# Performance work log

Hardware: AMD Instinct MI355X
Metric: run time of the kernel (lower is better)

The kernel has to match this reference:

```python
import jax, jax.numpy as jnp
import numpy as np

B, C, H, S, E, NH, DD, DS = 16, 256, 1024, 1024, 512, 8, 512, 64
HD = E // NH               # head dim = 64
REL_MAX = 2048             # seq_len + prediction_length
S1 = S + 1                 # dyn tokens + 1 static token
NEG = jnp.float32(-1e9)


def setup_inputs() -> dict:
    key = jax.random.key(0)
    ks = jax.random.split(key, 24)
    rn = lambda k, shp, s=0.02: (jax.random.normal(k, shp, jnp.float32) * s)
    return {
        # forward tensor args
        "x":      jax.random.normal(ks[0], (B, C, H), jnp.float32),
        "dyn":    jax.random.normal(ks[1], (B, S, DD), jnp.float32),
        "static": jax.random.normal(ks[2], (B, DS), jnp.float32),
        # dynamic/static encoders (nn.Linear: y = x @ W.T + b)
        "dyn_W":  rn(ks[3], (E, DD)),  "dyn_b":  jnp.zeros((E,), jnp.float32),
        "stat_W": rn(ks[4], (E, DS)),  "stat_b": jnp.zeros((E,), jnp.float32),
        # static FiLM MLP: Linear(E,E) -> LeakyReLU(0.1) -> Linear(E,C) -> Tanh
        "film_W1": rn(ks[5], (E, E)), "film_b1": jnp.zeros((E,), jnp.float32),
        "film_W2": rn(ks[6], (C, E)), "film_b2": jnp.zeros((C,), jnp.float32),
        # query_proj: Conv1d(C->E, k=1)  (weight stored as [E, C])
        "q_W": rn(ks[7], (E, C)), "q_b": jnp.zeros((E,), jnp.float32),
        # MultiheadAttention packed in-proj [3E, E] and out-proj [E, E]
        "in_proj_W": rn(ks[8], (3 * E, E)), "in_proj_b": jnp.zeros((3 * E,), jnp.float32),
        "out_W": rn(ks[9], (E, E)), "out_b": jnp.zeros((E,), jnp.float32),
        # context_proj: Conv1d(E->C, k=1) (weight stored as [C, E])
        "ctx_W": rn(ks[10], (C, E)), "ctx_b": jnp.zeros((C,), jnp.float32),
        # learned relative-position bias table, size 2*REL_MAX-1
        "bias_table": rn(ks[11], (2 * REL_MAX - 1,)),
    }


def _leaky(v):
    return jnp.where(v >= 0, v, 0.1 * v)


def _attn_mask(bias_table):
    """Fused relative-position bias + causal mask, shape [H, S1]."""
    q_ids = jnp.arange(H)[:, None]           # [H,1]
    k_ids = jnp.arange(S1)[None, :]          # [1,S1]
    rel = jnp.clip(q_ids - k_ids, -REL_MAX + 1, REL_MAX - 1)
    bias = bias_table[rel + REL_MAX - 1]     # [H,S1]
    # dynamic tokens: query q may attend dyn token j only if j <= min(q, S-1);
    # last (static) token always visible
    allowed = jnp.minimum(q_ids, S - 1)
    blocked = (k_ids < S) & (k_ids > allowed)
    return bias + jnp.where(blocked, NEG, 0.0)


def reference(x, dyn, static, dyn_W, dyn_b, stat_W, stat_b,
              film_W1, film_b1, film_W2, film_b2, q_W, q_b,
              in_proj_W, in_proj_b, out_W, out_b, ctx_W, ctx_b, bias_table):
    # encoders
    dyn_tokens = dyn @ dyn_W.T + dyn_b                      # [B,S,E]
    static_token = static @ stat_W.T + stat_b               # [B,E]
    film = jnp.tanh(_leaky(static_token @ film_W1.T + film_b1) @ film_W2.T + film_b2)  # [B,C]
    cond_tokens = jnp.concatenate([dyn_tokens, static_token[:, None, :]], axis=1)      # [B,S1,E]

    # query_proj (1x1 conv) : [B,C,H] -> [B,H,E]
    query = jnp.einsum('bch,ec->bhe', x, q_W) + q_b

    # multi-head cross-attention with additive mask
    Wq, Wk, Wv = in_proj_W[:E], in_proj_W[E:2 * E], in_proj_W[2 * E:]
    bq, bk, bv = in_proj_b[:E], in_proj_b[E:2 * E], in_proj_b[2 * E:]
    q = (query @ Wq.T + bq).reshape(B, H, NH, HD).transpose(0, 2, 1, 3)        # [B,NH,H,HD]
    k = (cond_tokens @ Wk.T + bk).reshape(B, S1, NH, HD).transpose(0, 2, 1, 3)  # [B,NH,S1,HD]
    v = (cond_tokens @ Wv.T + bv).reshape(B, S1, NH, HD).transpose(0, 2, 1, 3)

    mask = _attn_mask(bias_table)                                               # [H,S1]
    scores = jnp.einsum('bnqd,bnkd->bnqk', q, k) / jnp.sqrt(jnp.float32(HD)) + mask
    attn = jax.nn.softmax(scores, axis=-1)
    ctx = jnp.einsum('bnqk,bnkd->bnqd', attn, v)                                # [B,NH,H,HD]
    ctx = ctx.transpose(0, 2, 1, 3).reshape(B, H, E) @ out_W.T + out_b          # [B,H,E]

    cond_context = jnp.swapaxes(ctx, 1, 2)                                      # [B,E,H]
    cond_residual = jnp.einsum('beh,ce->bch', cond_context, ctx_W) + ctx_b[None, :, None]
    scale = (1.0 + film)[:, :, None]                                            # FiLM [B,C,1]
    x_cond = (x + cond_residual) * scale                                        # == x*s + res*s
    return x_cond
```

## Files before the change

kernel.cpp:

```cpp
#include <hip/hip_runtime.h>
#include <cmath>

#define B_  16
#define C_  256
#define H_  1024
#define S_  1024
#define E_  512
#define NH_ 8
#define DD_ 512
#define DS_ 64
#define HD_ 64
#define S1_ 1025
#define RELM 2048
#define SV  1032

typedef __attribute__((ext_vector_type(8))) short bf16x8;
typedef __attribute__((ext_vector_type(4))) float f32x4;

__device__ __forceinline__ unsigned short f2bf(float f) {
    unsigned u = __float_as_uint(f);
    u += 0x7fffu + ((u >> 16) & 1u);
    return (unsigned short)(u >> 16);
}

#if __has_builtin(__builtin_amdgcn_exp2f)
#define EXP2F(x) __builtin_amdgcn_exp2f(x)
#else
#define EXP2F(x) exp2f(x)
#endif

__device__ __forceinline__ void gl2lds16(const unsigned short* g, unsigned short* l) {
#if __has_builtin(__builtin_amdgcn_global_load_lds)
    __builtin_amdgcn_global_load_lds(
        (const __attribute__((address_space(1))) void*)g,
        (__attribute__((address_space(3))) void*)l, 16, 0, 0);
#else
    const int ln = threadIdx.x & 63;
    *(bf16x8*)(l + ln * 8) = *(const bf16x8*)g;
#endif
}

__device__ __forceinline__ void conv8(const float* __restrict__ src,
                                      unsigned short* __restrict__ dst, int i) {
    float4 a = *(const float4*)(src + i);
    float4 b = *(const float4*)(src + i + 4);
    bf16x8 o;
    ((unsigned short*)&o)[0] = f2bf(a.x); ((unsigned short*)&o)[1] = f2bf(a.y);
    ((unsigned short*)&o)[2] = f2bf(a.z); ((unsigned short*)&o)[3] = f2bf(a.w);
    ((unsigned short*)&o)[4] = f2bf(b.x); ((unsigned short*)&o)[5] = f2bf(b.y);
    ((unsigned short*)&o)[6] = f2bf(b.z); ((unsigned short*)&o)[7] = f2bf(b.w);
    *(bf16x8*)(dst + i) = o;
}

__device__ __forceinline__ float wred(float p) {
#pragma unroll
    for (int off = 32; off; off >>= 1) p += __shfl_down(p, off, 64);
    return p;
}

#define U_DYN 1048576
#define U_KV  1114112
#define U_Q   1146880
#define U_TOT 1163264
__global__ __launch_bounds__(512)
void prep_conv(const float* __restrict__ dyn, unsigned short* __restrict__ dyn16,
               const float* __restrict__ ipW, unsigned short* __restrict__ ipWq16,
               unsigned short* __restrict__ ipWkv16,
               const float* __restrict__ ctxW, unsigned short* __restrict__ ctxW16,
               const float* __restrict__ statIn,
               const float* __restrict__ stat_W, const float* __restrict__ stat_b,
               float* __restrict__ st_g, unsigned short* __restrict__ st16,
               const float* __restrict__ x, unsigned short* __restrict__ xT)
{
    __shared__ float tle[64][65];
    const int blk = blockIdx.x;
    const int t = threadIdx.x;
    if (blk < 512) {
        const float* ipWkv = ipW + (size_t)E_ * E_;
        const int stride = 512 * 512;
        for (int u = blk * 512 + t; u < U_TOT; u += stride) {
            if (u < U_DYN)      conv8(dyn,   dyn16,   u * 8);
            else if (u < U_KV)  conv8(ipWkv, ipWkv16, (u - U_DYN) * 8);
            else if (u < U_Q)   conv8(ipW,   ipWq16,  (u - U_KV) * 8);
            else                conv8(ctxW,  ctxW16,  (u - U_Q) * 8);
        }
    } else if (blk < 576) {
        const int sub = blk - 512;
        const int b = sub >> 2;
        const int q = sub & 3;
        const int wv = t >> 6;
        const int ln = t & 63;
        const float sv = statIn[b * DS_ + ln];
#pragma unroll 4
        for (int i = 0; i < 16; i++) {
            const int r = q * 128 + wv * 16 + i;
            const float p = wred(stat_W[(size_t)r * DS_ + ln] * sv);
            if (ln == 0) {
                const float v = p + stat_b[r];
                st_g[(size_t)b * E_ + r] = v;
                st16[(size_t)b * E_ + r] = f2bf(v);
            }
        }
    } else {
        const int sub = blk - 576;
        const int b  = sub >> 6;
        const int c0 = ((sub >> 4) & 3) * 64;
        const int h0 = (sub & 15) * 64;
        const int tx = t & 15, ty = t >> 4;
#pragma unroll
        for (int i = 0; i < 2; i++) {
            const float4 v = *(const float4*)&x[((size_t)(b * C_ + c0 + ty + i * 32)) * H_ + h0 + tx * 4];
            tle[ty + i * 32][tx * 4 + 0] = v.x;
            tle[ty + i * 32][tx * 4 + 1] = v.y;
            tle[ty + i * 32][tx * 4 + 2] = v.z;
            tle[ty + i * 32][tx * 4 + 3] = v.w;
        }
        __syncthreads();
#pragma unroll
        for (int i = 0; i < 2; i++) {
            const int hh = ty + i * 32;
            ushort4 o;
            o.x = f2bf(tle[tx * 4 + 0][hh]);
            o.y = f2bf(tle[tx * 4 + 1][hh]);
            o.z = f2bf(tle[tx * 4 + 2][hh]);
            o.w = f2bf(tle[tx * 4 + 3][hh]);
            *(ushort4*)&xT[((size_t)(b * H_ + h0 + hh)) * C_ + c0 + tx * 4] = o;
        }
    }
}

__global__ __launch_bounds__(512)
void prep_misc(const float* __restrict__ ipW, const float* __restrict__ ipb,
               const float* __restrict__ ctxW,
               const float* __restrict__ q_W, unsigned short* __restrict__ qWT16,
               const float* __restrict__ dynW, unsigned short* __restrict__ dynWT16,
               const float* __restrict__ outW, unsigned short* __restrict__ outWT16,
               const float* __restrict__ q_b, float* __restrict__ qb2,
               const float* __restrict__ dyn_b, float* __restrict__ bkv2,
               const float* __restrict__ out_b, const float* __restrict__ ctx_b,
               float* __restrict__ cb2,
               const float* __restrict__ st_g,
               const float* __restrict__ fW1, const float* __restrict__ fb1,
               float* __restrict__ h1_g)
{
    __shared__ float tle[64][65];
    const int blk = blockIdx.x;
    const int t = threadIdx.x;
    const float* ipWkv = ipW + (size_t)E_ * E_;
    const float* ipbkv = ipb + E_;

    if (blk < 128) {
        const int b   = blk >> 3;
        const int oct = blk & 7;
        const int wv  = t >> 6;
        const int ln  = t & 63;
        float str[8];
        *(float4*)&str[0] = *(const float4*)&st_g[(size_t)b * E_ + ln * 8];
        *(float4*)&str[4] = *(const float4*)&st_g[(size_t)b * E_ + ln * 8 + 4];
#pragma unroll 2
        for (int i = 0; i < 8; i++) {
            const int r = oct * 64 + wv * 8 + i;
            const float* wr = fW1 + (size_t)r * E_ + ln * 8;
            const float4 a = *(const float4*)wr;
            const float4 c = *(const float4*)(wr + 4);
            float p = a.x * str[0] + a.y * str[1] + a.z * str[2] + a.w * str[3]
                    + c.x * str[4] + c.y * str[5] + c.z * str[6] + c.w * str[7];
            p = wred(p);
            if (ln == 0) {
                const float v = p + fb1[r];
                h1_g[(size_t)b * E_ + r] = (v >= 0.f) ? v : 0.1f * v;
            }
        }
    } else if (blk < 352) {
        const int row = (blk - 128) * 8 + (t >> 6);
        const int ln  = t & 63;
        const float* src; const float* vec; float bias; float* dst;
        if (row < 512)       { src = ipW + (size_t)row * E_;            vec = q_b;   bias = ipb[row];        dst = qb2 + row; }
        else if (row < 1536) { const int n = row - 512;  src = ipWkv + (size_t)n * E_; vec = dyn_b; bias = ipbkv[n]; dst = bkv2 + n; }
        else                 { const int n = row - 1536; src = ctxW + (size_t)n * E_;  vec = out_b; bias = ctx_b[n]; dst = cb2 + n; }
        const float4 a  = *(const float4*)(src + ln * 8);
        const float4 c  = *(const float4*)(src + ln * 8 + 4);
        const float4 va = *(const float4*)(vec + ln * 8);
        const float4 vc = *(const float4*)(vec + ln * 8 + 4);
        float p = a.x * va.x + a.y * va.y + a.z * va.z + a.w * va.w
                + c.x * vc.x + c.y * vc.y + c.z * vc.z + c.w * vc.w;
        p = wred(p);
        if (ln == 0) *dst = p + bias;
    } else {
        const float* src; unsigned short* dst; int R, Cc, tile;
        const int tt = blk - 352;
        if (tt < 32)      { src = q_W;  dst = qWT16;   R = 512; Cc = 256; tile = tt; }
        else if (tt < 96) { src = dynW; dst = dynWT16; R = 512; Cc = 512; tile = tt - 32; }
        else              { src = outW; dst = outWT16; R = 512; Cc = 512; tile = tt - 96; }
        const int tpr = Cc / 64;
        const int r0 = (tile / tpr) * 64;
        const int c0 = (tile % tpr) * 64;
        const int tx = t & 15, ty = t >> 4;
#pragma unroll
        for (int i = 0; i < 2; i++) {
            const float4 v = *(const float4*)&src[(size_t)(r0 + ty + i * 32) * Cc + c0 + tx * 4];
            tle[ty + i * 32][tx * 4 + 0] = v.x;
            tle[ty + i * 32][tx * 4 + 1] = v.y;
            tle[ty + i * 32][tx * 4 + 2] = v.z;
            tle[ty + i * 32][tx * 4 + 3] = v.w;
        }
        __syncthreads();
#pragma unroll
        for (int i = 0; i < 2; i++) {
            const int cc = ty + i * 32;
            ushort4 o;
            o.x = f2bf(tle[tx * 4 + 0][cc]);
            o.y = f2bf(tle[tx * 4 + 1][cc]);
            o.z = f2bf(tle[tx * 4 + 2][cc]);
            o.w = f2bf(tle[tx * 4 + 3][cc]);
            *(ushort4*)&dst[(size_t)(c0 + cc) * R + r0 + tx * 4] = o;
        }
    }
}

__global__ __launch_bounds__(256)
void gemm_fold3(const unsigned short* __restrict__ ipWq16, const unsigned short* __restrict__ qWT16,
                unsigned short* __restrict__ WqW16,
                const unsigned short* __restrict__ ipWkv16, const unsigned short* __restrict__ dynWT16,
                unsigned short* __restrict__ Wkv216,
                const unsigned short* __restrict__ ctxW16, const unsigned short* __restrict__ outWT16,
                unsigned short* __restrict__ M216,
                const float* __restrict__ h1_g,
                const float* __restrict__ fW2, const float* __restrict__ fb2,
                float* __restrict__ scaleB)
{
    __shared__ unsigned short At[128 * 32];
    __shared__ unsigned short Wt[128 * 32];
    const int bid = blockIdx.x;
    const int tid  = threadIdx.x;
    if (bid >= 48) {
        const int sub = bid - 48;
        const int b = sub >> 2;
        const int q = sub & 3;
        const int wv = tid >> 6;
        const int ln = tid & 63;
        float h1r[8];
        *(float4*)&h1r[0] = *(const float4*)&h1_g[(size_t)b * E_ + ln * 8];
        *(float4*)&h1r[4] = *(const float4*)&h1_g[(size_t)b * E_ + ln * 8 + 4];
#pragma unroll 2
        for (int i = 0; i < 16; i++) {
            const int c = q * 64 + wv * 16 + i;
            const float* wr = fW2 + (size_t)c * E_ + ln * 8;
            const float4 a = *(const float4*)wr;
            const float4 cc = *(const float4*)(wr + 4);
            float p = a.x * h1r[0] + a.y * h1r[1] + a.z * h1r[2] + a.w * h1r[3]
                    + cc.x * h1r[4] + cc.y * h1r[5] + cc.z * h1r[6] + cc.w * h1r[7];
            p = wred(p);
            if (ln == 0) scaleB[b * C_ + c] = 1.f + tanhf(p + fb2[c]);
        }
        return;
    }
    const unsigned short *A, *W; unsigned short* O; int N, mb, nb;
    if (bid < 8)       { A = ipWq16;  W = qWT16;   O = WqW16;  N = 256; mb = bid >> 1;       nb = bid & 1; }
    else if (bid < 40) { A = ipWkv16; W = dynWT16; O = Wkv216; N = 512; mb = (bid - 8) >> 2; nb = (bid - 8) & 3; }
    else               { A = ctxW16;  W = outWT16; O = M216;   N = 512; mb = (bid - 40) >> 2; nb = (bid - 40) & 3; }
    const int m0 = mb * 128, n0 = nb * 128;

    const int wave = tid >> 6;
    const int lane = tid & 63;
    const int quad = lane >> 4;
    const int l15  = lane & 15;
    const int rw = (wave >> 1) * 64;
    const int cw = (wave & 1) * 64;
    const int srow = lane >> 2;
    const int scol = (lane & 3) * 8;

    f32x4 acc[4][4] = {};
    for (int k0 = 0; k0 < 512; k0 += 32) {
        __syncthreads();
#pragma unroll
        for (int c = 0; c < 2; c++) {
            const int chunk = wave + c * 4;
            gl2lds16(A + (size_t)(m0 + chunk * 16 + srow) * 512 + k0 + scol, &At[chunk * 512]);
            gl2lds16(W + (size_t)(n0 + chunk * 16 + srow) * 512 + k0 + scol, &Wt[chunk * 512]);
        }
        __syncthreads();
        bf16x8 af[4], wf[4];
#pragma unroll
        for (int i = 0; i < 4; i++)
            af[i] = *(const bf16x8*)&At[(rw + i * 16 + l15) * 32 + quad * 8];
#pragma unroll
        for (int j = 0; j < 4; j++)
            wf[j] = *(const bf16x8*)&Wt[(cw + j * 16 + l15) * 32 + quad * 8];
#pragma unroll
        for (int i = 0; i < 4; i++)
#pragma unroll
            for (int j = 0; j < 4; j++)
                acc[i][j] = __builtin_amdgcn_mfma_f32_16x16x32_bf16(af[i], wf[j], acc[i][j], 0, 0, 0);
    }
#pragma unroll
    for (int i = 0; i < 4; i++)
#pragma unroll
        for (int r = 0; r < 4; r++) {
            const int mm = m0 + rw + i * 16 + quad * 4 + r;
            unsigned short* cp = O + (size_t)mm * N + n0 + cw + l15;
#pragma unroll
            for (int j = 0; j < 4; j++)
                cp[j * 16] = f2bf(acc[i][j][r]);
        }
}

__global__ __launch_bounds__(256)
void gemm_qkv(const unsigned short* __restrict__ xT16, const unsigned short* __restrict__ WqW16,
              const float* __restrict__ qb2, unsigned short* __restrict__ q16,
              const unsigned short* __restrict__ dynA, const unsigned short* __restrict__ stA,
              const unsigned short* __restrict__ Wdyn, const unsigned short* __restrict__ Wst,
              const float* __restrict__ bdyn, const float* __restrict__ bst,
              unsigned short* __restrict__ k16, unsigned short* __restrict__ vtmp)
{
    __shared__ unsigned short At[2][128 * 32];
    __shared__ unsigned short Wt[2][128 * 32];
    const int bid0 = blockIdx.x;
    const int t = (bid0 & 7) * 193 + (bid0 >> 3);

    const int tid  = threadIdx.x;
    const int wave = tid >> 6;
    const int lane = tid & 63;
    const int quad = lane >> 4;
    const int l15  = lane & 15;
    const int rw = (wave >> 1) * 64;
    const int cw = (wave & 1) * 64;
    const int srow = lane >> 2;
    const int scol = (lane & 3) * 8;

    const unsigned short *A, *W;
    int m0, n0, K;
    bool isQ, stat = false;
    if (t < 1032) {
        const int y = t >> 3;
        stat = (y == 128);
        A = stat ? stA : dynA;
        W = stat ? Wst : Wdyn;
        m0 = stat ? 0 : y * 128;
        n0 = (t & 7) * 128;
        K = 512; isQ = false;
    } else {
        const int u = t - 1032;
        A = xT16; W = WqW16;
        m0 = (u >> 2) * 128;
        n0 = (u & 3) * 128;
        K = 256; isQ = true;
    }

    f32x4 acc[4][4] = {};
#pragma unroll
    for (int c = 0; c < 2; c++) {
        const int chunk = wave + c * 4;
        gl2lds16(A + (size_t)(m0 + chunk * 16 + srow) * K + scol, &At[0][chunk * 512]);
        gl2lds16(W + (size_t)(n0 + chunk * 16 + srow) * K + scol, &Wt[0][chunk * 512]);
    }
    int cur = 0;
    for (int k0 = 0; k0 < K; k0 += 32) {
        __syncthreads();
        if (k0 + 32 < K) {
            const int kn = k0 + 32;
#pragma unroll
            for (int c = 0; c < 2; c++) {
                const int chunk = wave + c * 4;
                gl2lds16(A + (size_t)(m0 + chunk * 16 + srow) * K + kn + scol, &At[cur ^ 1][chunk * 512]);
                gl2lds16(W + (size_t)(n0 + chunk * 16 + srow) * K + kn + scol, &Wt[cur ^ 1][chunk * 512]);
            }
        }
        bf16x8 af[4], wf[4];
#pragma unroll
        for (int i = 0; i < 4; i++)
            af[i] = *(const bf16x8*)&At[cur][(rw + i * 16 + l15) * 32 + quad * 8];
#pragma unroll
        for (int j = 0; j < 4; j++)
            wf[j] = *(const bf16x8*)&Wt[cur][(cw + j * 16 + l15) * 32 + quad * 8];
#pragma unroll
        for (int i = 0; i < 4; i++)
#pragma unroll
            for (int j = 0; j < 4; j++)
                acc[i][j] = __builtin_amdgcn_mfma_f32_16x16x32_bf16(af[i], wf[j], acc[i][j], 0, 0, 0);
        cur ^= 1;
    }

    if (isQ) {
        float bias4[4];
#pragma unroll
        for (int j = 0; j < 4; j++) bias4[j] = qb2[n0 + cw + j * 16 + l15];
#pragma unroll
        for (int i = 0; i < 4; i++) {
#pragma unroll
            for (int r = 0; r < 4; r++) {
                const int mm = m0 + rw + i * 16 + quad * 4 + r;
                unsigned short* cp = q16 + (size_t)mm * 512 + n0 + cw + l15;
#pragma unroll
                for (int j = 0; j < 4; j++)
                    cp[j * 16] = f2bf(acc[i][j][r] + bias4[j]);
            }
        }
    } else {
        const float* bias = stat ? bst : bdyn;
        const bool isV = (n0 >= 512);
        unsigned short* base = isV ? vtmp : k16;
        const int c0 = (isV ? n0 - 512 : n0) + cw + l15;
        float bias4[4];
#pragma unroll
        for (int j = 0; j < 4; j++) bias4[j] = bias[n0 + cw + j * 16 + l15];
#pragma unroll
        for (int i = 0; i < 4; i++) {
#pragma unroll
            for (int r = 0; r < 4; r++) {
                const int am = m0 + rw + i * 16 + quad * 4 + r;
                if (!stat || am < 16) {
                    const int orow = stat ? (am * S1_ + S_) : ((am >> 10) * S1_ + (am & 1023));
                    unsigned short* cp = base + (size_t)orow * 512 + c0;
#pragma unroll
                    for (int j = 0; j < 4; j++)
                        cp[j * 16] = f2bf(acc[i][j][r] + bias4[j]);
                }
            }
        }
    }
}

__global__ __launch_bounds__(256)
void gemm_final(const unsigned short* __restrict__ A, const unsigned short* __restrict__ W,
                const float* __restrict__ bias, float* __restrict__ Cout,
                const float* __restrict__ x, const float* __restrict__ scale)
{
    __shared__ unsigned short At[64 * 32];
    __shared__ unsigned short Wt[128 * 32];
    const int tid  = threadIdx.x;
    const int wave = tid >> 6;
    const int lane = tid & 63;
    const int quad = lane >> 4;
    const int l15  = lane & 15;
    const int m0 = blockIdx.y * 64;
    const int n0 = blockIdx.x * 128;
    const int rw = (wave >> 1) * 32;
    const int cw = (wave & 1) * 64;
    const int zb = blockIdx.z;
    const unsigned short* Wb = W + (size_t)zb * H_ * E_;

    const int srow = lane >> 2;
    const int scol = (lane & 3) * 8;

    f32x4 acc[2][4] = {};

    for (int k0 = 0; k0 < E_; k0 += 32) {
        __syncthreads();
        gl2lds16(A  + (size_t)(m0 + wave * 16 + srow) * E_ + k0 + scol, &At[wave * 512]);
#pragma unroll
        for (int c = 0; c < 2; c++) {
            const int chunk = wave + c * 4;
            gl2lds16(Wb + (size_t)(n0 + chunk * 16 + srow) * E_ + k0 + scol, &Wt[chunk * 512]);
        }
        __syncthreads();
        bf16x8 af[2], wf[4];
#pragma unroll
        for (int i = 0; i < 2; i++)
            af[i] = *(const bf16x8*)&At[(rw + i * 16 + l15) * 32 + quad * 8];
#pragma unroll
        for (int j = 0; j < 4; j++)
            wf[j] = *(const bf16x8*)&Wt[(cw + j * 16 + l15) * 32 + quad * 8];
#pragma unroll
        for (int i = 0; i < 2; i++)
#pragma unroll
            for (int j = 0; j < 4; j++)
                acc[i][j] = __builtin_amdgcn_mfma_f32_16x16x32_bf16(af[i], wf[j], acc[i][j], 0, 0, 0);
    }

#pragma unroll
    for (int i = 0; i < 2; i++) {
#pragma unroll
        for (int r = 0; r < 4; r++) {
            const int mm = m0 + rw + i * 16 + quad * 4 + r;
            const float cb = bias[mm];
            const float sc = scale[zb * C_ + mm];
            const size_t base = ((size_t)(zb * C_ + mm)) * H_ + n0 + cw + l15;
#pragma unroll
            for (int j = 0; j < 4; j++)
                Cout[base + j * 16] = (x[base + j * 16] + acc[i][j][r] + cb) * sc;
        }
    }
}

__global__ __launch_bounds__(256)
void vtrans_kernel(const unsigned short* __restrict__ vtmp, unsigned short* __restrict__ vT)
{
    __shared__ unsigned short tle[64][72];
    const int b = blockIdx.z;
    const int s0 = blockIdx.x * 64;
    const int d0 = blockIdx.y * 64;
    const int tx = threadIdx.x & 15;
    const int ty = threadIdx.x >> 4;
#pragma unroll
    for (int i = 0; i < 4; i++) {
        const int s = s0 + ty + i * 16;
        ushort4 v = {0, 0, 0, 0};
        if (s < S1_)
            v = *(const ushort4*)&vtmp[((size_t)(b * S1_ + s)) * 512 + d0 + tx * 4];
        tle[ty + i * 16][tx * 4 + 0] = v.x;
        tle[ty + i * 16][tx * 4 + 1] = v.y;
        tle[ty + i * 16][tx * 4 + 2] = v.z;
        tle[ty + i * 16][tx * 4 + 3] = v.w;
    }
    __syncthreads();
    if (s0 + tx * 4 < SV) {
#pragma unroll
        for (int i = 0; i < 4; i++) {
            const int dd = ty + i * 16;
            ushort4 o;
            o.x = tle[tx * 4 + 0][dd];
            o.y = tle[tx * 4 + 1][dd];
            o.z = tle[tx * 4 + 2][dd];
            o.w = tle[tx * 4 + 3][dd];
            *(ushort4*)&vT[((size_t)(b * 512 + d0 + dd)) * SV + s0 + tx * 4] = o;
        }
    }
}

#define KS 72
#define VTS 40
#define PS 40

__global__ __launch_bounds__(256)
void attn_mfma_kernel(const unsigned short* __restrict__ q,
                      const unsigned short* __restrict__ k16,
                      const unsigned short* __restrict__ vT,
                      const float* __restrict__ bt,
                      unsigned short* __restrict__ ctx)
{
    const int blk  = blockIdx.x;
    const int qt   = 7 - (blk >> 7);
    const int pair = blk & 127;
    const int nh   = pair & 7;
    const int b    = pair >> 3;
    const int tid  = threadIdx.x;
    const int wave = tid >> 6;
    const int lane = tid & 63;
    const int quad = lane >> 4;
    const int l15  = lane & 15;
    const int q0w  = qt * 128 + wave * 32;

    __shared__ unsigned short Kt[32 * KS];
    __shared__ unsigned short VTl[64 * VTS];
    __shared__ unsigned short Pt[4][16 * PS];
    __shared__ float btl[2048];

    for (int i = tid; i < 2048; i += 256)
        btl[i] = (i < 1024) ? -1.0e9f : bt[1023 + i] * 1.442695041f;

    const float c2 = 0.125f * 1.442695041f;

    bf16x8 qa[2][2];
    const size_t qbase = ((size_t)(b * H_ + q0w)) * E_ + nh * HD_;
#pragma unroll
    for (int qf = 0; qf < 2; qf++)
#pragma unroll
        for (int ch = 0; ch < 2; ch++)
            qa[qf][ch] = *(const bf16x8*)(q + qbase + (size_t)(qf * 16 + l15) * E_ + ch * 32 + quad * 8);

    bf16x8 ones;
#pragma unroll
    for (int j = 0; j < 8; j++) ((short*)&ones)[j] = (short)0x3F80;

    f32x4 o[2][4] = {};
    f32x4 lf[2] = {};
    bf16x8 pa[2];

    const int srow = tid >> 3;
    const int scol = (tid & 7) * 8;
    const int frow = tid >> 2;
    const int fcol = (tid & 3) * 8;
    const unsigned short* kbase = k16 + (size_t)(b * S1_) * 512 + nh * HD_;
    const unsigned short* vrow = vT + ((size_t)(b * 512 + nh * HD_ + frow)) * SV;
    const int ntiles = 4 * qt + 5;
    const int wblk0 = (l15 >> 3);
    const int wsub  = (l15 & 7);
    const int rblk  = (quad ^ ((l15 >> 2) & 3)) << 3;

    bf16x8 kreg = *(const bf16x8*)(kbase + (size_t)srow * 512 + scol);
    bf16x8 vreg = *(const bf16x8*)(vrow + fcol);

    for (int t = 0; t < ntiles; t++) {
        const int k0 = (t == ntiles - 1) ? 1024 : t * 32;
        __syncthreads();
        {
            *(bf16x8*)&Kt[srow * KS + scol] = kreg;
            *(bf16x8*)&VTl[frow * VTS + fcol] = vreg;
        }
        __syncthreads();
        if (t + 1 < ntiles) {
            const int nk0 = (t + 1 == ntiles - 1) ? 1024 : (t + 1) * 32;
            kreg = *(const bf16x8*)(kbase + (size_t)(nk0 + srow) * 512 + scol);
            vreg = *(const bf16x8*)(vrow + nk0 + fcol);
        }

        f32x4 s[2][2] = {};
        __builtin_amdgcn_s_setprio(1);
#pragma unroll
        for (int ch = 0; ch < 2; ch++) {
            const bf16x8 kb0 = *(const bf16x8*)&Kt[l15 * KS + ch * 32 + quad * 8];
            const bf16x8 kb1 = *(const bf16x8*)&Kt[(16 + l15) * KS + ch * 32 + quad * 8];
            s[0][0] = __builtin_amdgcn_mfma_f32_16x16x32_bf16(qa[0][ch], kb0, s[0][0], 0, 0, 0);
            s[1][0] = __builtin_amdgcn_mfma_f32_16x16x32_bf16(qa[1][ch], kb0, s[1][0], 0, 0, 0);
            s[0][1] = __builtin_amdgcn_mfma_f32_16x16x32_bf16(qa[0][ch], kb1, s[0][1], 0, 0, 0);
            s[1][1] = __builtin_amdgcn_mfma_f32_16x16x32_bf16(qa[1][ch], kb1, s[1][1], 0, 0, 0);
        }
        __builtin_amdgcn_s_setprio(0);

        if (t != ntiles - 1) {
#pragma unroll
            for (int qf = 0; qf < 2; qf++) {
                unsigned short* pw = Pt[wave];
#pragma unroll
                for (int f = 0; f < 2; f++) {
                    const int base = q0w + qf * 16 + quad * 4 - (k0 + f * 16 + l15) + 1024;
                    const int cswz = ((f * 2 + wblk0) ^ quad) * 8 + wsub;
#pragma unroll
                    for (int r = 0; r < 4; r++) {
                        const float pp = EXP2F(s[qf][f][r] * c2 + btl[base + r]);
                        pw[(quad * 4 + r) * PS + cswz] = f2bf(pp);
                    }
                }
                pa[qf] = *(const bf16x8*)&pw[l15 * PS + rblk];
            }
        } else {
#pragma unroll
            for (int qf = 0; qf < 2; qf++) {
                unsigned short* pw = Pt[wave];
#pragma unroll
                for (int f = 0; f < 2; f++) {
                    const int kk = k0 + f * 16 + l15;
                    const int cswz = ((f * 2 + wblk0) ^ quad) * 8 + wsub;
#pragma unroll
                    for (int r = 0; r < 4; r++) {
                        const int qi = q0w + qf * 16 + quad * 4 + r;
                        const float pp = (kk == 1024)
                            ? __expf(s[qf][f][r] * 0.125f + bt[1023 + qi]) : 0.f;
                        pw[(quad * 4 + r) * PS + cswz] = f2bf(pp);
                    }
                }
                pa[qf] = *(const bf16x8*)&pw[l15 * PS + rblk];
            }
        }

        __builtin_amdgcn_s_setprio(1);
#pragma unroll
        for (int qf = 0; qf < 2; qf++)
            lf[qf] = __builtin_amdgcn_mfma_f32_16x16x32_bf16(pa[qf], ones, lf[qf], 0, 0, 0);
#pragma unroll
        for (int dt = 0; dt < 4; dt++) {
            const bf16x8 vb = *(const bf16x8*)&VTl[(dt * 16 + l15) * VTS + quad * 8];
#pragma unroll
            for (int qf = 0; qf < 2; qf++)
                o[qf][dt] = __builtin_amdgcn_mfma_f32_16x16x32_bf16(pa[qf], vb, o[qf][dt], 0, 0, 0);
        }
        __builtin_amdgcn_s_setprio(0);
    }

#pragma unroll
    for (int qf = 0; qf < 2; qf++) {
        unsigned short* crow = ctx + ((size_t)(b * H_ + q0w + qf * 16 + quad * 4)) * E_ + nh * HD_ + l15;
#pragma unroll
        for (int r = 0; r < 4; r++) {
            const float inv = 1.f / lf[qf][r];
#pragma unroll
            for (int dt = 0; dt < 4; dt++)
                crow[(size_t)r * E_ + dt * 16] = f2bf(o[qf][dt][r] * inv);
        }
    }
}

extern "C" void kernel_launch(void* const* d_in, const int* in_sizes, int n_in,
                              void* d_out, int out_size, void* d_ws, size_t ws_size,
                              hipStream_t stream)
{
    (void)in_sizes; (void)n_in; (void)out_size; (void)ws_size;
    const float* x      = (const float*)d_in[0];
    const float* dyn    = (const float*)d_in[1];
    const float* statIn = (const float*)d_in[2];
    const float* dyn_W  = (const float*)d_in[3];
    const float* dyn_b  = (const float*)d_in[4];
    const float* stat_W = (const float*)d_in[5];
    const float* stat_b = (const float*)d_in[6];
    const float* fW1    = (const float*)d_in[7];
    const float* fb1    = (const float*)d_in[8];
    const float* fW2    = (const float*)d_in[9];
    const float* fb2    = (const float*)d_in[10];
    const float* q_W    = (const float*)d_in[11];
    const float* q_b    = (const float*)d_in[12];
    const float* ipW    = (const float*)d_in[13];
    const float* ipb    = (const float*)d_in[14];
    const float* out_W  = (const float*)d_in[15];
    const float* out_b  = (const float*)d_in[16];
    const float* ctx_W  = (const float*)d_in[17];
    const float* ctx_b  = (const float*)d_in[18];
    const float* bt     = (const float*)d_in[19];
    float* out = (float*)d_out;
    const float* ipbkv = ipb + E_;

    const size_t KV_ROWS = 16512;
    char* w = (char*)d_ws; size_t off = 0;
    unsigned short* k16   = (unsigned short*)(w + off); off += KV_ROWS * 512 * 2;
    unsigned short* vtmp  = (unsigned short*)(w + off); off += KV_ROWS * 512 * 2;
    unsigned short* dyn16 = (unsigned short*)(w + off); off += (size_t)16 * 512 * SV * 2;
    unsigned short* q16   = (unsigned short*)(w + off); off += (size_t)B_ * H_ * E_ * 2;
    unsigned short* xT16  = (unsigned short*)(w + off); off += (size_t)B_ * H_ * C_ * 2;
    unsigned short* st16    = (unsigned short*)(w + off); off += (size_t)128 * E_ * 2;
    unsigned short* Wkv216  = (unsigned short*)(w + off); off += (size_t)1024 * 512 * 2;
    unsigned short* ipWkv16 = (unsigned short*)(w + off); off += (size_t)1024 * 512 * 2;
    unsigned short* ipWq16  = (unsigned short*)(w + off); off += (size_t)512 * 512 * 2;
    unsigned short* ctxW16  = (unsigned short*)(w + off); off += (size_t)256 * 512 * 2;
    unsigned short* qWT16   = (unsigned short*)(w + off); off += (size_t)256 * 512 * 2;
    unsigned short* dynWT16 = (unsigned short*)(w + off); off += (size_t)512 * 512 * 2;
    unsigned short* outWT16 = (unsigned short*)(w + off); off += (size_t)512 * 512 * 2;
    unsigned short* WqW16   = (unsigned short*)(w + off); off += (size_t)E_ * C_ * 2;
    unsigned short* M216    = (unsigned short*)(w + off); off += (size_t)C_ * E_ * 2;
    float* scaleB = (float*)(w + off); off += (size_t)B_ * C_ * 4;
    float* qb2    = (float*)(w + off); off += E_ * 4;
    float* bkv2   = (float*)(w + off); off += 1024 * 4;
    float* cb2    = (float*)(w + off); off += C_ * 4;
    float* st_g   = (float*)(w + off); off += (size_t)B_ * E_ * 4;
    float* h1_g   = (float*)(w + off); off += (size_t)B_ * E_ * 4;
    unsigned short* vT16  = dyn16;
    unsigned short* ctx16 = vtmp;

    prep_conv<<<1600, 512, 0, stream>>>(dyn, dyn16, ipW, ipWq16, ipWkv16, ctx_W, ctxW16,
                                        statIn, stat_W, stat_b, st_g, st16, x, xT16);
    prep_misc<<<512, 512, 0, stream>>>(ipW, ipb, ctx_W, q_W, qWT16, dyn_W, dynWT16,
                                       out_W, outWT16, q_b, qb2, dyn_b, bkv2,
                                       out_b, ctx_b, cb2,
                                       st_g, fW1, fb1, h1_g);
    gemm_fold3<<<112, 256, 0, stream>>>(ipWq16, qWT16, WqW16,
                                        ipWkv16, dynWT16, Wkv216,
                                        ctxW16, outWT16, M216,
                                        h1_g, fW2, fb2, scaleB);
    gemm_qkv<<<1544, 256, 0, stream>>>(xT16, WqW16, qb2, q16,
                                       dyn16, st16, Wkv216, ipWkv16, bkv2, ipbkv,
                                       k16, vtmp);
    vtrans_kernel<<<dim3(17, 8, B_), 256, 0, stream>>>(vtmp, vT16);
    attn_mfma_kernel<<<1024, 256, 0, stream>>>(q16, k16, vT16, bt, ctx16);
    gemm_final<<<dim3(H_ / 128, C_ / 64, B_), 256, 0, stream>>>(
        M216, ctx16, cb2, out, x, scaleB);
}
```

Before: 265.4 us.

## Merge prep_misc into neighbouring kernels and shift FiLM stages down the pipeline

Removes the prep_misc launch. Its bias-fold and weight-transpose blocks move into prep_conv, the FiLM first layer moves into gemm_fold3 as extra blocks, and the FiLM second layer moves into gemm_qkv as extra blocks. The goal is to cut one kernel launch and its inter-kernel gap by rebalancing the dependency chain across stages. In exchange, the extra blocks in gemm_fold3 and gemm_qkv may add tail work, and those kernels now carry more branches.

Result: no change. 260.4 us (-1.9%).

```diff
diff --git a/kernel.cpp b/kernel.cpp
--- a/kernel.cpp
+++ b/kernel.cpp
@@ -64,19 +64,27 @@
 #define U_TOT 1163264
 __global__ __launch_bounds__(512)
 void prep_conv(const float* __restrict__ dyn, unsigned short* __restrict__ dyn16,
-               const float* __restrict__ ipW, unsigned short* __restrict__ ipWq16,
-               unsigned short* __restrict__ ipWkv16,
+               const float* __restrict__ ipW, const float* __restrict__ ipb,
+               unsigned short* __restrict__ ipWq16, unsigned short* __restrict__ ipWkv16,
                const float* __restrict__ ctxW, unsigned short* __restrict__ ctxW16,
                const float* __restrict__ statIn,
                const float* __restrict__ stat_W, const float* __restrict__ stat_b,
                float* __restrict__ st_g, unsigned short* __restrict__ st16,
-               const float* __restrict__ x, unsigned short* __restrict__ xT)
+               const float* __restrict__ x, unsigned short* __restrict__ xT,
+               const float* __restrict__ q_W, unsigned short* __restrict__ qWT16,
+               const float* __restrict__ dynW, unsigned short* __restrict__ dynWT16,
+               const float* __restrict__ outW, unsigned short* __restrict__ outWT16,
+               const float* __restrict__ q_b, float* __restrict__ qb2,
+               const float* __restrict__ dyn_b, float* __restrict__ bkv2,
+               const float* __restrict__ out_b, const float* __restrict__ ctx_b,
+               float* __restrict__ cb2)
 {
     __shared__ float tle[64][65];
     const int blk = blockIdx.x;
     const int t = threadIdx.x;
+    const float* ipWkv = ipW + (size_t)E_ * E_;
+    const float* ipbkv = ipb + E_;
     if (blk < 512) {
-        const float* ipWkv = ipW + (size_t)E_ * E_;
         const int stride = 512 * 512;
         for (int u = blk * 512 + t; u < U_TOT; u += stride) {
             if (u < U_DYN)      conv8(dyn,   dyn16,   u * 8);
@@ -101,7 +109,7 @@
                 st16[(size_t)b * E_ + r] = f2bf(v);
             }
         }
-    } else {
+    } else if (blk < 1600) {
         const int sub = blk - 576;
         const int b  = sub >> 6;
         const int c0 = ((sub >> 4) & 3) * 64;
@@ -126,53 +134,8 @@
             o.w = f2bf(tle[tx * 4 + 3][hh]);
             *(ushort4*)&xT[((size_t)(b * H_ + h0 + hh)) * C_ + c0 + tx * 4] = o;
         }
-    }
-}
-
-__global__ __launch_bounds__(512)
-void prep_misc(const float* __restrict__ ipW, const float* __restrict__ ipb,
-               const float* __restrict__ ctxW,
-               const float* __restrict__ q_W, unsigned short* __restrict__ qWT16,
-               const float* __restrict__ dynW, unsigned short* __restrict__ dynWT16,
-               const float* __restrict__ outW, unsigned short* __restrict__ outWT16,
-               const float* __restrict__ q_b, float* __restrict__ qb2,
-               const float* __restrict__ dyn_b, float* __restrict__ bkv2,
-               const float* __restrict__ out_b, const float* __restrict__ ctx_b,
-               float* __restrict__ cb2,
-               const float* __restrict__ st_g,
-               const float* __restrict__ fW1, const float* __restrict__ fb1,
-               float* __restrict__ h1_g)
-{
-    __shared__ float tle[64][65];
-    const int blk = blockIdx.x;
-    const int t = threadIdx.x;
-    const float* ipWkv = ipW + (size_t)E_ * E_;
-    const float* ipbkv = ipb + E_;
-
-    if (blk < 128) {
-        const int b   = blk >> 3;
-        const int oct = blk & 7;
-        const int wv  = t >> 6;
-        const int ln  = t & 63;
-        float str[8];
-        *(float4*)&str[0] = *(const float4*)&st_g[(size_t)b * E_ + ln * 8];
-        *(float4*)&str[4] = *(const float4*)&st_g[(size_t)b * E_ + ln * 8 + 4];
-#pragma unroll 2
-        for (int i = 0; i < 8; i++) {
-            const int r = oct * 64 + wv * 8 + i;
-            const float* wr = fW1 + (size_t)r * E_ + ln * 8;
-            const float4 a = *(const float4*)wr;
-            const float4 c = *(const float4*)(wr + 4);
-            float p = a.x * str[0] + a.y * str[1] + a.z * str[2] + a.w * str[3]
-                    + c.x * str[4] + c.y * str[5] + c.z * str[6] + c.w * str[7];
-            p = wred(p);
-            if (ln == 0) {
-                const float v = p + fb1[r];
-                h1_g[(size_t)b * E_ + r] = (v >= 0.f) ? v : 0.1f * v;
-            }
-        }
-    } else if (blk < 352) {
-        const int row = (blk - 128) * 8 + (t >> 6);
+    } else if (blk < 1824) {
+        const int row = (blk - 1600) * 8 + (t >> 6);
         const int ln  = t & 63;
         const float* src; const float* vec; float bias; float* dst;
         if (row < 512)       { src = ipW + (size_t)row * E_;            vec = q_b;   bias = ipb[row];        dst = qb2 + row; }
@@ -188,7 +151,7 @@
         if (ln == 0) *dst = p + bias;
     } else {
         const float* src; unsigned short* dst; int R, Cc, tile;
-        const int tt = blk - 352;
+        const int tt = blk - 1824;
         if (tt < 32)      { src = q_W;  dst = qWT16;   R = 512; Cc = 256; tile = tt; }
         else if (tt < 96) { src = dynW; dst = dynWT16; R = 512; Cc = 512; tile = tt - 32; }
         else              { src = outW; dst = outWT16; R = 512; Cc = 512; tile = tt - 96; }
@@ -225,9 +188,9 @@
                 unsigned short* __restrict__ Wkv216,
                 const unsigned short* __restrict__ ctxW16, const unsigned short* __restrict__ outWT16,
                 unsigned short* __restrict__ M216,
-                const float* __restrict__ h1_g,
-                const float* __restrict__ fW2, const float* __restrict__ fb2,
-                float* __restrict__ scaleB)
+                const float* __restrict__ st_g,
+                const float* __restrict__ fW1, const float* __restrict__ fb1,
+                float* __restrict__ h1_g)
 {
     __shared__ unsigned short At[128 * 32];
     __shared__ unsigned short Wt[128 * 32];
@@ -235,6 +198,96 @@
     const int tid  = threadIdx.x;
     if (bid >= 48) {
         const int sub = bid - 48;
+        const int b   = sub >> 3;
+        const int oct = sub & 7;
+        const int wv  = tid >> 6;
+        const int ln  = tid & 63;
+        float str[8];
+        *(float4*)&str[0] = *(const float4*)&st_g[(size_t)b * E_ + ln * 8];
+        *(float4*)&str[4] = *(const float4*)&st_g[(size_t)b * E_ + ln * 8 + 4];
+#pragma unroll 2
+        for (int i = 0; i < 16; i++) {
+            const int r = oct * 64 + wv * 16 + i;
+            const float* wr = fW1 + (size_t)r * E_ + ln * 8;
+            const float4 a = *(const float4*)wr;
+            const float4 c = *(const float4*)(wr + 4);
+            float p = a.x * str[0] + a.y * str[1] + a.z * str[2] + a.w * str[3]
+                    + c.x * str[4] + c.y * str[5] + c.z * str[6] + c.w * str[7];
+            p = wred(p);
+            if (ln == 0) {
+                const float v = p + fb1[r];
+                h1_g[(size_t)b * E_ + r] = (v >= 0.f) ? v : 0.1f * v;
+            }
+        }
+        return;
+    }
+    const unsigned short *A, *W; unsigned short* O; int N, mb, nb;
+    if (bid < 8)       { A = ipWq16;  W = qWT16;   O = WqW16;  N = 256; mb = bid >> 1;       nb = bid & 1; }
+    else if (bid < 40) { A = ipWkv16; W = dynWT16; O = Wkv216; N = 512; mb = (bid - 8) >> 2; nb = (bid - 8) & 3; }
+    else               { A = ctxW16;  W = outWT16; O = M216;   N = 512; mb = (bid - 40) >> 2; nb = (bid - 40) & 3; }
+    const int m0 = mb * 128, n0 = nb * 128;
+
+    const int wave = tid >> 6;
+    const int lane = tid & 63;
+    const int quad = lane >> 4;
+    const int l15  = lane & 15;
+    const int rw = (wave >> 1) * 64;
+    const int cw = (wave & 1) * 64;
+    const int srow = lane >> 2;
+    const int scol = (lane & 3) * 8;
+
+    f32x4 acc[4][4] = {};
+    for (int k0 = 0; k0 < 512; k0 += 32) {
+        __syncthreads();
+#pragma unroll
+        for (int c = 0; c < 2; c++) {
+            const int chunk = wave + c * 4;
+            gl2lds16(A + (size_t)(m0 + chunk * 16 + srow) * 512 + k0 + scol, &At[chunk * 512]);
+            gl2lds16(W + (size_t)(n0 + chunk * 16 + srow) * 512 + k0 + scol, &Wt[chunk * 512]);
+        }
+        __syncthreads();
+        bf16x8 af[4], wf[4];
+#pragma unroll
+        for (int i = 0; i < 4; i++)
+            af[i] = *(const bf16x8*)&At[(rw + i * 16 + l15) * 32 + quad * 8];
+#pragma unroll
+        for (int j = 0; j < 4; j++)
+            wf[j] = *(const bf16x8*)&Wt[(cw + j * 16 + l15) * 32 + quad * 8];
+#pragma unroll
+        for (int i = 0; i < 4; i++)
+#pragma unroll
+            for (int j = 0; j < 4; j++)
+                acc[i][j] = __builtin_amdgcn_mfma_f32_16x16x32_bf16(af[i], wf[j], acc[i][j], 0, 0, 0);
+    }
+#pragma unroll
+    for (int i = 0; i < 4; i++)
+#pragma unroll
+        for (int r = 0; r < 4; r++) {
+            const int mm = m0 + rw + i * 16 + quad * 4 + r;
+            unsigned short* cp = O + (size_t)mm * N + n0 + cw + l15;
+#pragma unroll
+            for (int j = 0; j < 4; j++)
+                cp[j * 16] = f2bf(acc[i][j][r]);
+        }
+}
+
+__global__ __launch_bounds__(256)
+void gemm_qkv(const unsigned short* __restrict__ xT16, const unsigned short* __restrict__ WqW16,
+              const float* __restrict__ qb2, unsigned short* __restrict__ q16,
+              const unsigned short* __restrict__ dynA, const unsigned short* __restrict__ stA,
+              const unsigned short* __restrict__ Wdyn, const unsigned short* __restrict__ Wst,
+              const float* __restrict__ bdyn, const float* __restrict__ bst,
+              unsigned short* __restrict__ k16, unsigned short* __restrict__ vtmp,
+              const float* __restrict__ h1_g,
+              const float* __restrict__ fW2, const float* __restrict__ fb2,
+              float* __restrict__ scaleB)
+{
+    __shared__ unsigned short At[2][128 * 32];
+    __shared__ unsigned short Wt[2][128 * 32];
+    const int bid0 = blockIdx.x;
+    const int tid  = threadIdx.x;
+    if (bid0 >= 1544) {
+        const int sub = bid0 - 1544;
         const int b = sub >> 2;
         const int q = sub & 3;
         const int wv = tid >> 6;
@@ -255,70 +308,8 @@
         }
         return;
     }
-    const unsigned short *A, *W; unsigned short* O; int N, mb, nb;
-    if (bid < 8)       { A = ipWq16;  W = qWT16;   O = WqW16;  N = 256; mb = bid >> 1;       nb = bid & 1; }
-    else if (bid < 40) { A = ipWkv16; W = dynWT16; O = Wkv216; N = 512; mb = (bid - 8) >> 2; nb = (bid - 8) & 3; }
-    else               { A = ctxW16;  W = outWT16; O = M216;   N = 512; mb = (bid - 40) >> 2; nb = (bid - 40) & 3; }
-    const int m0 = mb * 128, n0 = nb * 128;
-
-    const int wave = tid >> 6;
-    const int lane = tid & 63;
-    const int quad = lane >> 4;
-    const int l15  = lane & 15;
-    const int rw = (wave >> 1) * 64;
-    const int cw = (wave & 1) * 64;
-    const int srow = lane >> 2;
-    const int scol = (lane & 3) * 8;
-
-    f32x4 acc[4][4] = {};
-    for (int k0 = 0; k0 < 512; k0 += 32) {
-        __syncthreads();
-#pragma unroll
-        for (int c = 0; c < 2; c++) {
-            const int chunk = wave + c * 4;
-            gl2lds16(A + (size_t)(m0 + chunk * 16 + srow) * 512 + k0 + scol, &At[chunk * 512]);
-            gl2lds16(W + (size_t)(n0 + chunk * 16 + srow) * 512 + k0 + scol, &Wt[chunk * 512]);
-        }
-        __syncthreads();
-        bf16x8 af[4], wf[4];
-#pragma unroll
-        for (int i = 0; i < 4; i++)
-            af[i] = *(const bf16x8*)&At[(rw + i * 16 + l15) * 32 + quad * 8];
-#pragma unroll
-        for (int j = 0; j < 4; j++)
-            wf[j] = *(const bf16x8*)&Wt[(cw + j * 16 + l15) * 32 + quad * 8];
-#pragma unroll
-        for (int i = 0; i < 4; i++)
-#pragma unroll
-            for (int j = 0; j < 4; j++)
-                acc[i][j] = __builtin_amdgcn_mfma_f32_16x16x32_bf16(af[i], wf[j], acc[i][j], 0, 0, 0);
-    }
-#pragma unroll
-    for (int i = 0; i < 4; i++)
-#pragma unroll
-        for (int r = 0; r < 4; r++) {
-            const int mm = m0 + rw + i * 16 + quad * 4 + r;
-            unsigned short* cp = O + (size_t)mm * N + n0 + cw + l15;
-#pragma unroll
-            for (int j = 0; j < 4; j++)
-                cp[j * 16] = f2bf(acc[i][j][r]);
-        }
-}
-
-__global__ __launch_bounds__(256)
-void gemm_qkv(const unsigned short* __restrict__ xT16, const unsigned short* __restrict__ WqW16,
-              const float* __restrict__ qb2, unsigned short* __restrict__ q16,
-              const unsigned short* __restrict__ dynA, const unsigned short* __restrict__ stA,
-              const unsigned short* __restrict__ Wdyn, const unsigned short* __restrict__ Wst,
-              const float* __restrict__ bdyn, const float* __restrict__ bst,
-              unsigned short* __restrict__ k16, unsigned short* __restrict__ vtmp)
-{
-    __shared__ unsigned short At[2][128 * 32];
-    __shared__ unsigned short Wt[2][128 * 32];
-    const int bid0 = blockIdx.x;
     const int t = (bid0 & 7) * 193 + (bid0 >> 3);
 
-    const int tid  = threadIdx.x;
     const int wave = tid >> 6;
     const int lane = tid & 63;
     const int quad = lane >> 4;
@@ -725,19 +716,18 @@
     unsigned short* vT16  = dyn16;
     unsigned short* ctx16 = vtmp;
 
-    prep_conv<<<1600, 512, 0, stream>>>(dyn, dyn16, ipW, ipWq16, ipWkv16, ctx_W, ctxW16,
-                                        statIn, stat_W, stat_b, st_g, st16, x, xT16);
-    prep_misc<<<512, 512, 0, stream>>>(ipW, ipb, ctx_W, q_W, qWT16, dyn_W, dynWT16,
-                                       out_W, outWT16, q_b, qb2, dyn_b, bkv2,
-                                       out_b, ctx_b, cb2,
-                                       st_g, fW1, fb1, h1_g);
-    gemm_fold3<<<112, 256, 0, stream>>>(ipWq16, qWT16, WqW16,
+    prep_conv<<<1984, 512, 0, stream>>>(dyn, dyn16, ipW, ipb, ipWq16, ipWkv16,
+                                        ctx_W, ctxW16, statIn, stat_W, stat_b,
+                                        st_g, st16, x, xT16,
+                                        q_W, qWT16, dyn_W, dynWT16, out_W, outWT16,
+                                        q_b, qb2, dyn_b, bkv2, out_b, ctx_b, cb2);
+    gemm_fold3<<<176, 256, 0, stream>>>(ipWq16, qWT16, WqW16,
                                         ipWkv16, dynWT16, Wkv216,
                                         ctxW16, outWT16, M216,
-                                        h1_g, fW2, fb2, scaleB);
-    gemm_qkv<<<1544, 256, 0, stream>>>(xT16, WqW16, qb2, q16,
+                                        st_g, fW1, fb1, h1_g);
+    gemm_qkv<<<1608, 256, 0, stream>>>(xT16, WqW16, qb2, q16,
                                        dyn16, st16, Wkv216, ipWkv16, bkv2, ipbkv,
-                                       k16, vtmp);
+                                       k16, vtmp, h1_g, fW2, fb2, scaleB);
     vtrans_kernel<<<dim3(17, 8, B_), 256, 0, stream>>>(vtmp, vT16);
     attn_mfma_kernel<<<1024, 256, 0, stream>>>(q16, k16, vT16, bt, ctx16);
     gemm_final<<<dim3(H_ / 128, C_ / 64, B_), 256, 0, stream>>>(
```
